# Kernel optimization log

Measured on AMD Instinct MI355X. Metric: run time of the kernel, lower is better.

The kernel has to match this reference:

```python
import jax, jax.numpy as jnp
import numpy as np

D_MODEL = 768
NUM_HEADS = 12
HEAD_DIM = D_MODEL // NUM_HEADS


def setup_inputs() -> dict:
    key = jax.random.key(0)
    ks = jax.random.split(key, 9)
    B, S = 2, 2048
    s = 1.0 / np.sqrt(D_MODEL)
    x = jax.random.normal(ks[0], (B, S, D_MODEL), dtype=jnp.float32)
    Wq = jax.random.normal(ks[1], (D_MODEL, D_MODEL), dtype=jnp.float32) * s
    Wk = jax.random.normal(ks[2], (D_MODEL, D_MODEL), dtype=jnp.float32) * s
    Wv = jax.random.normal(ks[3], (D_MODEL, D_MODEL), dtype=jnp.float32) * s
    Wo = jax.random.normal(ks[4], (D_MODEL, D_MODEL), dtype=jnp.float32) * s
    bq = jax.random.normal(ks[5], (D_MODEL,), dtype=jnp.float32) * 0.01
    bk = jax.random.normal(ks[6], (D_MODEL,), dtype=jnp.float32) * 0.01
    bv = jax.random.normal(ks[7], (D_MODEL,), dtype=jnp.float32) * 0.01
    bo = jax.random.normal(ks[8], (D_MODEL,), dtype=jnp.float32) * 0.01
    return {"x": x, "Wq": Wq, "bq": bq, "Wk": Wk, "bk": bk,
            "Wv": Wv, "bv": bv, "Wo": Wo, "bo": bo}


def reference(x, Wq, bq, Wk, bk, Wv, bv, Wo, bo):
    B, S, _ = x.shape
    # projections; reshape to [B, H, S, Dh]
    def split_heads(t):
        return t.reshape(B, S, NUM_HEADS, HEAD_DIM).transpose(0, 2, 1, 3)
    q = split_heads(x @ Wq + bq)
    k = split_heads(x @ Wk + bk)
    v = split_heads(x @ Wv + bv)
    scale = 1.0 / np.sqrt(HEAD_DIM)
    scores = jnp.einsum("bhqd,bhkd->bhqk", q, k) * scale  # [B,H,S,S]
    attn = jax.nn.softmax(scores, axis=-1)
    # dropout p=0.0 (eval) -> identity
    ctx = jnp.einsum("bhqk,bhkd->bhqd", attn, v)
    ctx = ctx.transpose(0, 2, 1, 3).reshape(B, S, D_MODEL)
    return ctx @ Wo + bo
```

## Files before the change

### kernel.cpp

```cpp
#include <hip/hip_runtime.h>
#include <hip/hip_bf16.h>
#include <hip/hip_fp16.h>

#define D_MODEL 768
#define NHEADS  12
#define HD      64
#define BATCH   2
#define SEQ     2048
#define NTOK    (BATCH*SEQ)
#define NX      ((size_t)NTOK * D_MODEL)
#define NW      ((size_t)D_MODEL * D_MODEL)
#define SC_LOG2 0.18033688f

typedef __attribute__((ext_vector_type(8))) short    short8;
typedef __attribute__((ext_vector_type(8))) _Float16 half8;
typedef __attribute__((ext_vector_type(4))) float    f32x4;

__device__ __forceinline__ float bf2f(short s) {
    union { unsigned u; float f; } c;
    c.u = ((unsigned)(unsigned short)s) << 16;
    return c.f;
}
__device__ __forceinline__ short f2bf(float f) {
    __hip_bfloat16 h = __float2bfloat16(f);
    return *(short*)&h;
}

#ifdef __has_builtin
#if __has_builtin(__builtin_amdgcn_global_load_lds)
#define HAS_GLD 1
#endif
#endif
#ifdef HAS_GLD
#define GLD16(gp, lp) __builtin_amdgcn_global_load_lds( \
    (const __attribute__((address_space(1))) void*)(gp), \
    (__attribute__((address_space(3))) void*)(lp), 16, 0, 0)
#endif

__global__ __launch_bounds__(256) void fused_conv(
        const void* __restrict__ xin,
        const void* __restrict__ w0, const void* __restrict__ w1,
        const void* __restrict__ w2, const void* __restrict__ w3,
        const void* __restrict__ b0, const void* __restrict__ b1,
        const void* __restrict__ b2, const void* __restrict__ b3,
        short* __restrict__ xc, short* __restrict__ wt,
        short* __restrict__ bc, int* __restrict__ flag)
{
    __shared__ int red[256];
    __shared__ float T[64][65];
    const int tid = threadIdx.x;
    const int F = blockIdx.x;

    {
        const short* xs = (const short*)xin;
        int maxe = 0;
#pragma unroll
        for (int u = 0; u < 16; ++u) {
            int e = ((unsigned short)xs[tid * 16 + u] >> 7) & 0xFF;
            maxe = max(maxe, e);
        }
        red[tid] = maxe;
        __syncthreads();
        for (int s = 128; s > 0; s >>= 1) {
            if (tid < s) red[tid] = max(red[tid], red[tid + s]);
            __syncthreads();
        }
    }
    const bool isf = (red[0] > 140);

    if (F < 3072) {
        const int i = F * 256 + tid;
        if (isf) {
            float4 f = ((const float4*)xin)[i];
            short4 o = { f2bf(f.x), f2bf(f.y), f2bf(f.z), f2bf(f.w) };
            ((short4*)xc)[i] = o;
        } else {
            ((short4*)xc)[i] = ((const short4*)xin)[i];
        }
    } else if (F < 3648) {
        const int G = F - 3072;
        const int z = G / 144, rr = G % 144;
        const int k0 = (rr % 12) * 64, n0 = (rr / 12) * 64;
        const void* src = (z == 0) ? w0 : (z == 1) ? w1 : (z == 2) ? w2 : w3;
        const float sc = (z == 0) ? SC_LOG2 : 1.0f;
        const int la = tid & 15, lb = tid >> 4;
#pragma unroll
        for (int u = 0; u < 4; ++u) {
            const int kr = (lb & 3) + 4 * u + 16 * (lb >> 2);
            if (isf) {
                float4 f = *(const float4*)((const float*)src + (size_t)(k0 + kr) * D_MODEL + n0 + la * 4);
                T[kr][la*4+0] = f.x; T[kr][la*4+1] = f.y; T[kr][la*4+2] = f.z; T[kr][la*4+3] = f.w;
            } else {
                short4 s = *(const short4*)((const short*)src + (size_t)(k0 + kr) * D_MODEL + n0 + la * 4);
                T[kr][la*4+0] = bf2f(s.x); T[kr][la*4+1] = bf2f(s.y);
                T[kr][la*4+2] = bf2f(s.z); T[kr][la*4+3] = bf2f(s.w);
            }
        }
        __syncthreads();
#pragma unroll
        for (int u = 0; u < 4; ++u) {
            const int nr = (lb & 3) + 4 * u + 16 * (lb >> 2);
            short4 o = { f2bf(T[la*4+0][nr] * sc), f2bf(T[la*4+1][nr] * sc),
                         f2bf(T[la*4+2][nr] * sc), f2bf(T[la*4+3][nr] * sc) };
            *(short4*)(wt + (size_t)z * NW + (size_t)(n0 + nr) * D_MODEL + k0 + la * 4) = o;
        }
    } else {
        if (tid == 0) *flag = isf ? 1 : 0;
        const void* srcs[4] = { b0, b1, b2, b3 };
        for (int z = 0; z < 4; ++z) {
            const float sc = (z == 0) ? SC_LOG2 : 1.0f;
            for (int i = tid; i < D_MODEL; i += 256) {
                float v = isf ? ((const float*)srcs[z])[i] : bf2f(((const short*)srcs[z])[i]);
                bc[z * D_MODEL + i] = f2bf(v * sc);
            }
        }
    }
}

__global__ __launch_bounds__(256) void qkv_gemm(const short* __restrict__ X,
                                                const short* __restrict__ Wt,
                                                const short* __restrict__ bias,
                                                short* __restrict__ qb,
                                                short* __restrict__ kb,
                                                _Float16* __restrict__ Vt)
{
    __shared__ __align__(16) char shbuf[32768];
    short* Als = (short*)shbuf;
    short* Bls = (short*)(shbuf + 16384);
    _Float16* T = (_Float16*)shbuf;

    const int tid = threadIdx.x;
    const int wave = tid >> 6, lane = tid & 63;
    const int quad = lane >> 4, l16 = lane & 15;
    const int wm = wave & 1, wn = wave >> 1;
    const int m0 = blockIdx.x * 128;
    const int ng = blockIdx.y * 128;

    f32x4 acc[4][4];
#pragma unroll
    for (int nt = 0; nt < 4; ++nt) {
        const float bv = bf2f(bias[ng + wn*64 + nt*16 + l16]);
#pragma unroll
        for (int mt = 0; mt < 4; ++mt) acc[mt][nt] = (f32x4){bv, bv, bv, bv};
    }

    const int row = tid >> 2, ch = (tid & 3) * 8;
#ifdef HAS_GLD
#define QSTAGE(buf, k0) do { \
        GLD16(X  + (size_t)(m0 + row)      * D_MODEL + (k0) + ch, &Als[(buf)*4096 + tid*8]); \
        GLD16(X  + (size_t)(m0 + 64 + row) * D_MODEL + (k0) + ch, &Als[(buf)*4096 + 2048 + tid*8]); \
        GLD16(Wt + (size_t)(ng + row)      * D_MODEL + (k0) + ch, &Bls[(buf)*4096 + tid*8]); \
        GLD16(Wt + (size_t)(ng + 64 + row) * D_MODEL + (k0) + ch, &Bls[(buf)*4096 + 2048 + tid*8]); \
    } while (0)
#else
#define QSTAGE(buf, k0) do { \
        short8 r0 = *(const short8*)(X  + (size_t)(m0 + row)      * D_MODEL + (k0) + ch); \
        short8 r1 = *(const short8*)(X  + (size_t)(m0 + 64 + row) * D_MODEL + (k0) + ch); \
        short8 r2 = *(const short8*)(Wt + (size_t)(ng + row)      * D_MODEL + (k0) + ch); \
        short8 r3 = *(const short8*)(Wt + (size_t)(ng + 64 + row) * D_MODEL + (k0) + ch); \
        *(short8*)&Als[(buf)*4096 + tid*8] = r0;  *(short8*)&Als[(buf)*4096 + 2048 + tid*8] = r1; \
        *(short8*)&Bls[(buf)*4096 + tid*8] = r2;  *(short8*)&Bls[(buf)*4096 + 2048 + tid*8] = r3; \
    } while (0)
#endif

    QSTAGE(0, 0);
    __syncthreads();

    for (int ks = 0; ks < 24; ++ks) {
        const int cur = ks & 1;
        if (ks + 1 < 24) QSTAGE(cur ^ 1, (ks + 1) * 32);

        short8 a[4], b[4];
#pragma unroll
        for (int mt = 0; mt < 4; ++mt)
            a[mt] = *(const short8*)&Als[cur*4096 + (wm*64 + mt*16 + l16) * 32 + quad*8];
#pragma unroll
        for (int nt = 0; nt < 4; ++nt)
            b[nt] = *(const short8*)&Bls[cur*4096 + (wn*64 + nt*16 + l16) * 32 + quad*8];
#pragma unroll
        for (int mt = 0; mt < 4; ++mt)
#pragma unroll
        for (int nt = 0; nt < 4; ++nt)
            acc[mt][nt] = __builtin_amdgcn_mfma_f32_16x16x32_bf16(a[mt], b[nt], acc[mt][nt], 0, 0, 0);

        __syncthreads();
    }
#undef QSTAGE

    const int seg = blockIdx.y / 6;
    if (seg < 2) {
        short* out = seg ? kb : qb;
        const int nl = ng - seg * 768;
#pragma unroll
        for (int mt = 0; mt < 4; ++mt)
#pragma unroll
        for (int nt = 0; nt < 4; ++nt) {
            const int n = nl + wn*64 + nt*16 + l16;
#pragma unroll
            for (int r = 0; r < 4; ++r) {
                const int m = m0 + wm*64 + mt*16 + quad*4 + r;
                out[(size_t)m * D_MODEL + n] = f2bf(acc[mt][nt][r]);
            }
        }
    } else {
        const int batch = m0 >> 11, tokb = m0 & (SEQ - 1);
        for (int pass = 0; pass < 2; ++pass) {
            if (wn == pass) {
#pragma unroll
                for (int nt = 0; nt < 4; ++nt) {
                    const int dim_l = nt*16 + l16;
#pragma unroll
                    for (int mt = 0; mt < 4; ++mt) {
                        const int tok_l = wm*64 + mt*16 + quad*4;
                        union { _Float16 h4[4]; int2 v; } u;
#pragma unroll
                        for (int r = 0; r < 4; ++r) u.h4[r] = (_Float16)acc[mt][nt][r];
                        *(int2*)&T[dim_l * 136 + tok_l] = u.v;
                    }
                }
            }
            __syncthreads();
#pragma unroll
            for (int u = 0; u < 4; ++u) {
                const int slot = tid + u * 256;
                const int drow = slot >> 4, chk = slot & 15;
                int4 val = *(const int4*)&T[drow * 136 + chk * 8];
                const int dim_g = ng - 1536 + pass*64 + drow;
                const int h = dim_g >> 6, d = dim_g & 63;
                *(int4*)(Vt + ((size_t)(batch * NHEADS + h) * HD + d) * SEQ + tokb + chk*8) = val;
            }
            if (pass == 0) __syncthreads();
        }
    }
}

__global__ __launch_bounds__(256) void out_gemm(const short* __restrict__ X,
                                                const short* __restrict__ Wt,
                                                const short* __restrict__ bias,
                                                void* __restrict__ outv,
                                                const int* __restrict__ flag)
{
    __shared__ short Als[2][2048];
    __shared__ short Bls[2][2048];

    const int tid = threadIdx.x;
    const int wave = tid >> 6, lane = tid & 63;
    const int quad = lane >> 4, l16 = lane & 15;
    const int m0 = blockIdx.x * 64;
    const int n0 = blockIdx.y * 64;

    f32x4 acc[4];
#pragma unroll
    for (int nt = 0; nt < 4; ++nt) {
        const float bv = bf2f(bias[n0 + nt*16 + l16]);
        acc[nt] = (f32x4){bv, bv, bv, bv};
    }

    const int row = tid >> 2, ch = (tid & 3) * 8;
#ifdef HAS_GLD
#define OSTAGE(buf, k0) do { \
        GLD16(X  + (size_t)(m0 + row) * D_MODEL + (k0) + ch, &Als[buf][tid*8]); \
        GLD16(Wt + (size_t)(n0 + row) * D_MODEL + (k0) + ch, &Bls[buf][tid*8]); \
    } while (0)
#else
#define OSTAGE(buf, k0) do { \
        short8 r0 = *(const short8*)(X  + (size_t)(m0 + row) * D_MODEL + (k0) + ch); \
        short8 r1 = *(const short8*)(Wt + (size_t)(n0 + row) * D_MODEL + (k0) + ch); \
        *(short8*)&Als[buf][tid*8] = r0; \
        *(short8*)&Bls[buf][tid*8] = r1; \
    } while (0)
#endif

    OSTAGE(0, 0);
    __syncthreads();

    for (int ks = 0; ks < 24; ++ks) {
        const int cur = ks & 1;
        if (ks + 1 < 24) OSTAGE(cur ^ 1, (ks + 1) * 32);

        short8 a = *(const short8*)&Als[cur][(wave*16 + l16) * 32 + quad*8];
#pragma unroll
        for (int nt = 0; nt < 4; ++nt) {
            short8 b = *(const short8*)&Bls[cur][(nt*16 + l16) * 32 + quad*8];
            acc[nt] = __builtin_amdgcn_mfma_f32_16x16x32_bf16(a, b, acc[nt], 0, 0, 0);
        }
        __syncthreads();
    }
#undef OSTAGE

    const bool outf32 = (*flag != 0);
#pragma unroll
    for (int nt = 0; nt < 4; ++nt) {
        const int n = n0 + nt*16 + l16;
#pragma unroll
        for (int r = 0; r < 4; ++r) {
            const int m = m0 + wave*16 + quad*4 + r;
            const size_t idx = (size_t)m * D_MODEL + n;
            if (outf32) ((float*)outv)[idx] = acc[nt][r];
            else        ((short*)outv)[idx] = f2bf(acc[nt][r]);
        }
    }
}

__global__ __launch_bounds__(256) void attn_mfma(const short* __restrict__ q,
                                                 const short* __restrict__ k,
                                                 const _Float16* __restrict__ Vt,
                                                 short* __restrict__ ctx)
{
    __shared__ short    Kls[2][64 * 64];
    __shared__ _Float16 Vls[2][64 * 64];
    __shared__ _Float16 Pls[4][16 * 64];

    const int tid  = threadIdx.x;
    const int wave = tid >> 6, lane = tid & 63;
    const int quad = lane >> 4, l16 = lane & 15;

    const int F = blockIdx.x;
    const int xcd = F & 7, slot = F >> 3;
    const int bh = xcd * 3 + (slot >> 5);
    const int q0 = (slot & 31) * 64;
    const int b = bh / NHEADS, h = bh % NHEADS;
    const size_t bS = (size_t)b * SEQ;
    const int myq = q0 + wave * 16 + l16;

    short8 qf[2];
#pragma unroll
    for (int k0h = 0; k0h < 2; ++k0h)
        qf[k0h] = *(const short8*)(q + (bS + myq) * D_MODEL + h*HD + k0h*32 + quad*8);

    half8 ones;
#pragma unroll
    for (int j = 0; j < 8; ++j) ones[j] = (_Float16)1.0f;

    const int s0 = tid, s1 = tid + 256;
    const int kr0 = s0 >> 3, kc0 = (s0 & 7) ^ (kr0 & 7);
    const int kr1 = s1 >> 3, kc1 = (s1 & 7) ^ (kr1 & 7);
    const short*    kg0 = k  + (bS + kr0) * D_MODEL + h*HD + kc0*8;
    const short*    kg1 = k  + (bS + kr1) * D_MODEL + h*HD + kc1*8;
    const _Float16* vg0 = Vt + ((size_t)bh * HD + kr0) * SEQ + kc0*8;
    const _Float16* vg1 = Vt + ((size_t)bh * HD + kr1) * SEQ + kc1*8;

#ifdef HAS_GLD
#define STAGE(buf, j0) do { \
        GLD16(kg0 + (size_t)(j0) * D_MODEL, &Kls[buf][s0 * 8]); \
        GLD16(kg1 + (size_t)(j0) * D_MODEL, &Kls[buf][s1 * 8]); \
        GLD16(vg0 + (j0),                   &Vls[buf][s0 * 8]); \
        GLD16(vg1 + (j0),                   &Vls[buf][s1 * 8]); \
    } while (0)
#else
#define STAGE(buf, j0) do { \
        short8 a_ = *(const short8*)(kg0 + (size_t)(j0) * D_MODEL); \
        short8 b_ = *(const short8*)(kg1 + (size_t)(j0) * D_MODEL); \
        half8  c_ = *(const half8*)(vg0 + (j0)); \
        half8  d_ = *(const half8*)(vg1 + (j0)); \
        *(short8*)&Kls[buf][s0 * 8] = a_;  *(short8*)&Kls[buf][s1 * 8] = b_; \
        *(half8*)&Vls[buf][s0 * 8] = c_;   *(half8*)&Vls[buf][s1 * 8] = d_; \
    } while (0)
#endif

    float m_ = -1e30f;
    f32x4 lacc = (f32x4){0.f, 0.f, 0.f, 0.f};
    f32x4 o[4];
#pragma unroll
    for (int t = 0; t < 4; ++t) o[t] = (f32x4){0.f, 0.f, 0.f, 0.f};

    STAGE(0, 0);
    __syncthreads();

    for (int jt = 0; jt < SEQ / 64; ++jt) {
        const int cur = jt & 1;
        if (jt + 1 < SEQ / 64) STAGE(cur ^ 1, (jt + 1) * 64);

        f32x4 s4[4];
#pragma unroll
        for (int t = 0; t < 4; ++t) s4[t] = (f32x4){0.f, 0.f, 0.f, 0.f};
#pragma unroll
        for (int k0h = 0; k0h < 2; ++k0h)
#pragma unroll
        for (int t = 0; t < 4; ++t) {
            const int krow = t*16 + l16;
            short8 kf = *(const short8*)&Kls[cur][krow*64 + (((k0h*4 + quad) ^ (krow & 7)) * 8)];
            s4[t] = __builtin_amdgcn_mfma_f32_16x16x32_bf16(kf, qf[k0h], s4[t], 0, 0, 0);
        }

        float mx = s4[0][0];
#pragma unroll
        for (int t = 0; t < 4; ++t)
#pragma unroll
        for (int r = 0; r < 4; ++r) mx = fmaxf(mx, s4[t][r]);
#pragma unroll
        for (int d = 1; d < 64; d <<= 1) mx = fmaxf(mx, __shfl_xor(mx, d));
        const float mn = fmaxf(m_, mx);
        if (__builtin_amdgcn_readfirstlane((int)(mn > m_))) {
            const float al = exp2f(m_ - mn);
#pragma unroll
            for (int t = 0; t < 4; ++t) {
                o[t][0] *= al; o[t][1] *= al; o[t][2] *= al; o[t][3] *= al;
            }
            lacc[0] *= al; lacc[1] *= al; lacc[2] *= al; lacc[3] *= al;
            m_ = mn;
        }

#pragma unroll
        for (int t = 0; t < 4; ++t) {
            union { _Float16 h4[4]; int2 v; } u4;
#pragma unroll
            for (int r = 0; r < 4; ++r) u4.h4[r] = (_Float16)exp2f(s4[t][r] - mn);
            const int c = (t*2 + (quad >> 1)) ^ (l16 & 7);
            *(int2*)&Pls[wave][l16*64 + c*8 + (quad & 1)*4] = u4.v;
        }

#pragma unroll
        for (int k0h = 0; k0h < 2; ++k0h) {
            const int pc = (k0h*4 + quad) ^ (l16 & 7);
            half8 pf = *(half8*)&Pls[wave][l16*64 + pc*8];
            lacc = __builtin_amdgcn_mfma_f32_16x16x32_f16(ones, pf, lacc, 0, 0, 0);
#pragma unroll
            for (int t = 0; t < 4; ++t) {
                const int vrow = t*16 + l16;
                half8 vf = *(const half8*)&Vls[cur][vrow*64 + (((k0h*4 + quad) ^ (vrow & 7)) * 8)];
                o[t] = __builtin_amdgcn_mfma_f32_16x16x32_f16(vf, pf, o[t], 0, 0, 0);
            }
        }

        __syncthreads();
    }

    const float inv = 1.0f / lacc[0];
    const size_t rowp = (bS + myq) * D_MODEL + h*HD;
#pragma unroll
    for (int t = 0; t < 4; ++t) {
        union { short s4v[4]; int2 v; } u4;
#pragma unroll
        for (int r = 0; r < 4; ++r) u4.s4v[r] = f2bf(o[t][r] * inv);
        *(int2*)(ctx + rowp + t*16 + quad*4) = u4.v;
    }
#undef STAGE
}

extern "C" void kernel_launch(void* const* d_in, const int* in_sizes, int n_in,
                              void* d_out, int out_size, void* d_ws, size_t ws_size,
                              hipStream_t stream)
{
    int* flag = (int*)d_ws;
    short* xc = (short*)((char*)d_ws + 64);
    short* Wt = xc + NX;
    short* bc = Wt + 4 * NW;
    short* qb = bc + 4 * D_MODEL;
    short* kb = qb + NX;
    _Float16* Vt = (_Float16*)(kb + NX);
    short* cb = (short*)(Vt + NX);

    fused_conv<<<3649, 256, 0, stream>>>(d_in[0],
                                         d_in[1], d_in[3], d_in[5], d_in[7],
                                         d_in[2], d_in[4], d_in[6], d_in[8],
                                         xc, Wt, bc, flag);

    qkv_gemm<<<dim3(NTOK/128, 2304/128), 256, 0, stream>>>(xc, Wt, bc, qb, kb, Vt);

    attn_mfma<<<768, 256, 0, stream>>>(qb, kb, Vt, cb);

    out_gemm<<<dim3(NTOK/64, D_MODEL/64), 256, 0, stream>>>(cb, Wt + 3*NW, bc + 3*D_MODEL, d_out, flag);
}
```

Baseline: 195.1 us.

## Split key tiles across wave pairs and reuse K/V fragments over two query groups

Each pair of waves now shares 32 queries, and each wave processes half of every 64-key tile, so every K and V fragment read from LDS feeds two MFMAs instead of one. A final merge step rescales the two partial softmax states through shared memory and writes the context rows. The cross-lane max reduction is now skipped when no lane's max rose. The aim is to cut LDS fragment traffic per MFMA. The cost is a cross-wave merge epilogue that reuses the K buffer as float scratch, and that scratch is larger than Kls alone, so it relies on Vls being laid out right after it.

```diff
diff --git a/kernel.cpp b/kernel.cpp
--- a/kernel.cpp
+++ b/kernel.cpp
@@ -302,14 +302,16 @@
     }
 }
 
+#define PROW 40
 __global__ __launch_bounds__(256) void attn_mfma(const short* __restrict__ q,
                                                  const short* __restrict__ k,
                                                  const _Float16* __restrict__ Vt,
                                                  short* __restrict__ ctx)
 {
-    __shared__ short    Kls[2][64 * 64];
-    __shared__ _Float16 Vls[2][64 * 64];
-    __shared__ _Float16 Pls[4][16 * 64];
+    __shared__ short    Kls[2][4096];
+    __shared__ _Float16 Vls[2][4096];
+    __shared__ _Float16 Pw[4][32 * PROW];
+    __shared__ float    Ml[4][32][2];
 
     const int tid  = threadIdx.x;
     const int wave = tid >> 6, lane = tid & 63;
@@ -321,12 +323,18 @@
     const int q0 = (slot & 31) * 64;
     const int b = bh / NHEADS, h = bh % NHEADS;
     const size_t bS = (size_t)b * SEQ;
-    const int myq = q0 + wave * 16 + l16;
-
-    short8 qf[2];
+
+    const int pairq = wave >> 1;
+    const int kh    = wave & 1;
+    const int qbase = q0 + pairq * 32;
+
+    short8 qf[2][2];
+#pragma unroll
+    for (int qg = 0; qg < 2; ++qg)
 #pragma unroll
     for (int k0h = 0; k0h < 2; ++k0h)
-        qf[k0h] = *(const short8*)(q + (bS + myq) * D_MODEL + h*HD + k0h*32 + quad*8);
+        qf[qg][k0h] = *(const short8*)(q + (bS + qbase + qg*16 + l16) * D_MODEL
+                                         + h*HD + k0h*32 + quad*8);
 
     half8 ones;
 #pragma unroll
@@ -359,10 +367,14 @@
 #endif
 
     float m_ = -1e30f;
-    f32x4 lacc = (f32x4){0.f, 0.f, 0.f, 0.f};
-    f32x4 o[4];
-#pragma unroll
-    for (int t = 0; t < 4; ++t) o[t] = (f32x4){0.f, 0.f, 0.f, 0.f};
+    f32x4 lacc[2];
+    f32x4 o[2][4];
+#pragma unroll
+    for (int qg = 0; qg < 2; ++qg) {
+        lacc[qg] = (f32x4){0.f, 0.f, 0.f, 0.f};
+#pragma unroll
+        for (int t = 0; t < 4; ++t) o[qg][t] = (f32x4){0.f, 0.f, 0.f, 0.f};
+    }
 
     STAGE(0, 0);
     __syncthreads();
@@ -371,69 +383,112 @@
         const int cur = jt & 1;
         if (jt + 1 < SEQ / 64) STAGE(cur ^ 1, (jt + 1) * 64);
 
-        f32x4 s4[4];
-#pragma unroll
-        for (int t = 0; t < 4; ++t) s4[t] = (f32x4){0.f, 0.f, 0.f, 0.f};
+        f32x4 s4[2][2];
+#pragma unroll
+        for (int qg = 0; qg < 2; ++qg)
+#pragma unroll
+        for (int t = 0; t < 2; ++t) s4[qg][t] = (f32x4){0.f, 0.f, 0.f, 0.f};
 #pragma unroll
         for (int k0h = 0; k0h < 2; ++k0h)
 #pragma unroll
+        for (int t = 0; t < 2; ++t) {
+            const int krow = kh*32 + t*16 + l16;
+            short8 kf = *(const short8*)&Kls[cur][krow*64 + (((k0h*4 + quad) ^ (krow & 7)) * 8)];
+#pragma unroll
+            for (int qg = 0; qg < 2; ++qg)
+                s4[qg][t] = __builtin_amdgcn_mfma_f32_16x16x32_bf16(kf, qf[qg][k0h], s4[qg][t], 0, 0, 0);
+        }
+
+        float mx = s4[0][0][0];
+#pragma unroll
+        for (int qg = 0; qg < 2; ++qg)
+#pragma unroll
+        for (int t = 0; t < 2; ++t)
+#pragma unroll
+        for (int r = 0; r < 4; ++r) mx = fmaxf(mx, s4[qg][t][r]);
+        if (__any(mx > m_)) {
+#pragma unroll
+            for (int d = 1; d < 64; d <<= 1) mx = fmaxf(mx, __shfl_xor(mx, d));
+            const float mn = fmaxf(m_, mx);
+            const float al = exp2f(m_ - mn);
+#pragma unroll
+            for (int qg = 0; qg < 2; ++qg) {
+#pragma unroll
+                for (int t = 0; t < 4; ++t) {
+                    o[qg][t][0] *= al; o[qg][t][1] *= al;
+                    o[qg][t][2] *= al; o[qg][t][3] *= al;
+                }
+                lacc[qg][0] *= al; lacc[qg][1] *= al;
+                lacc[qg][2] *= al; lacc[qg][3] *= al;
+            }
+            m_ = mn;
+        }
+
+#pragma unroll
+        for (int qg = 0; qg < 2; ++qg)
+#pragma unroll
+        for (int t = 0; t < 2; ++t) {
+            union { _Float16 h4[4]; int2 v; } u4;
+#pragma unroll
+            for (int r = 0; r < 4; ++r) u4.h4[r] = (_Float16)exp2f(s4[qg][t][r] - m_);
+            *(int2*)&Pw[wave][(qg*16 + l16) * PROW + t*16 + quad*4] = u4.v;
+        }
+
+        half8 pf[2];
+#pragma unroll
+        for (int qg = 0; qg < 2; ++qg) {
+            pf[qg] = *(half8*)&Pw[wave][(qg*16 + l16) * PROW + quad*8];
+            lacc[qg] = __builtin_amdgcn_mfma_f32_16x16x32_f16(ones, pf[qg], lacc[qg], 0, 0, 0);
+        }
+#pragma unroll
         for (int t = 0; t < 4; ++t) {
-            const int krow = t*16 + l16;
-            short8 kf = *(const short8*)&Kls[cur][krow*64 + (((k0h*4 + quad) ^ (krow & 7)) * 8)];
-            s4[t] = __builtin_amdgcn_mfma_f32_16x16x32_bf16(kf, qf[k0h], s4[t], 0, 0, 0);
-        }
-
-        float mx = s4[0][0];
+            const int vrow = t*16 + l16;
+            half8 vf = *(const half8*)&Vls[cur][vrow*64 + (((kh*4 + quad) ^ (vrow & 7)) * 8)];
+#pragma unroll
+            for (int qg = 0; qg < 2; ++qg)
+                o[qg][t] = __builtin_amdgcn_mfma_f32_16x16x32_f16(vf, pf[qg], o[qg][t], 0, 0, 0);
+        }
+
+        __syncthreads();
+    }
+
+    float* Ow = (float*)&Kls[0][0];
+#pragma unroll
+    for (int qg = 0; qg < 2; ++qg) {
 #pragma unroll
         for (int t = 0; t < 4; ++t)
-#pragma unroll
-        for (int r = 0; r < 4; ++r) mx = fmaxf(mx, s4[t][r]);
-#pragma unroll
-        for (int d = 1; d < 64; d <<= 1) mx = fmaxf(mx, __shfl_xor(mx, d));
-        const float mn = fmaxf(m_, mx);
-        if (__builtin_amdgcn_readfirstlane((int)(mn > m_))) {
-            const float al = exp2f(m_ - mn);
-#pragma unroll
-            for (int t = 0; t < 4; ++t) {
-                o[t][0] *= al; o[t][1] *= al; o[t][2] *= al; o[t][3] *= al;
-            }
-            lacc[0] *= al; lacc[1] *= al; lacc[2] *= al; lacc[3] *= al;
-            m_ = mn;
-        }
-
-#pragma unroll
-        for (int t = 0; t < 4; ++t) {
-            union { _Float16 h4[4]; int2 v; } u4;
-#pragma unroll
-            for (int r = 0; r < 4; ++r) u4.h4[r] = (_Float16)exp2f(s4[t][r] - mn);
-            const int c = (t*2 + (quad >> 1)) ^ (l16 & 7);
-            *(int2*)&Pls[wave][l16*64 + c*8 + (quad & 1)*4] = u4.v;
-        }
-
-#pragma unroll
-        for (int k0h = 0; k0h < 2; ++k0h) {
-            const int pc = (k0h*4 + quad) ^ (l16 & 7);
-            half8 pf = *(half8*)&Pls[wave][l16*64 + pc*8];
-            lacc = __builtin_amdgcn_mfma_f32_16x16x32_f16(ones, pf, lacc, 0, 0, 0);
-#pragma unroll
-            for (int t = 0; t < 4; ++t) {
-                const int vrow = t*16 + l16;
-                half8 vf = *(const half8*)&Vls[cur][vrow*64 + (((k0h*4 + quad) ^ (vrow & 7)) * 8)];
-                o[t] = __builtin_amdgcn_mfma_f32_16x16x32_f16(vf, pf, o[t], 0, 0, 0);
-            }
-        }
-
-        __syncthreads();
-    }
-
-    const float inv = 1.0f / lacc[0];
-    const size_t rowp = (bS + myq) * D_MODEL + h*HD;
-#pragma unroll
-    for (int t = 0; t < 4; ++t) {
-        union { short s4v[4]; int2 v; } u4;
-#pragma unroll
-        for (int r = 0; r < 4; ++r) u4.s4v[r] = f2bf(o[t][r] * inv);
-        *(int2*)(ctx + rowp + t*16 + quad*4) = u4.v;
+            *(f32x4*)&Ow[(wave*32 + qg*16 + l16) * 64 + t*16 + quad*4] = o[qg][t];
+        if (quad == 0) {
+            Ml[wave][qg*16 + l16][0] = m_;
+            Ml[wave][qg*16 + l16][1] = lacc[qg][0];
+        }
+    }
+    __syncthreads();
+
+    {
+        const int qg2 = tid >> 2;
+        const int seg = tid & 3;
+        const int pr  = qg2 >> 5, ql = qg2 & 31;
+        const int wa = pr*2, wb = wa + 1;
+        const float ma = Ml[wa][ql][0], la = Ml[wa][ql][1];
+        const float mb = Ml[wb][ql][0], lb = Ml[wb][ql][1];
+        const float M = fmaxf(ma, mb);
+        const float sa = exp2f(ma - M), sb = exp2f(mb - M);
+        const float inv = 1.0f / (la * sa + lb * sb);
+        union { short s8[8]; int4 v; } u0, u1;
+#pragma unroll
+        for (int i = 0; i < 4; ++i) {
+            f32x4 oa = *(const f32x4*)&Ow[(wa*32 + ql) * 64 + seg*16 + i*4];
+            f32x4 ob = *(const f32x4*)&Ow[(wb*32 + ql) * 64 + seg*16 + i*4];
+#pragma unroll
+            for (int r = 0; r < 4; ++r) {
+                const short v = f2bf((oa[r] * sa + ob[r] * sb) * inv);
+                if (i < 2) u0.s8[i*4 + r] = v; else u1.s8[(i-2)*4 + r] = v;
+            }
+        }
+        short* cp = ctx + (bS + q0 + qg2) * D_MODEL + h*HD + seg*16;
+        *(int4*)cp = u0.v;
+        *(int4*)(cp + 8) = u1.v;
     }
 #undef STAGE
 }
```

Result: slower. 216.0 us (+10.7%).

## Fuse x fp32-to-bf16 conversion into QKV GEMM A-tile loads

Applied to the files above, without the earlier changes.

Removes the separate x conversion pass from the prep kernel, which shrinks it from 3649 to 577 blocks and drops the xc workspace buffer. The QKV GEMM now reads the raw input, converting fp32 to bf16 in registers when the flag says the input is float, and writes the A tile to LDS after the MFMAs of each step. This avoids a full write and reread of the converted activation. In exchange, each GEMM block rereads fp32 x (twice the bytes) across all 18 N-blocks, and the A tile can no longer use direct global-to-LDS loads.

```diff
diff --git a/kernel.cpp b/kernel.cpp
--- a/kernel.cpp
+++ b/kernel.cpp
@@ -43,8 +43,7 @@
         const void* __restrict__ w2, const void* __restrict__ w3,
         const void* __restrict__ b0, const void* __restrict__ b1,
         const void* __restrict__ b2, const void* __restrict__ b3,
-        short* __restrict__ xc, short* __restrict__ wt,
-        short* __restrict__ bc, int* __restrict__ flag)
+        short* __restrict__ wt, short* __restrict__ bc, int* __restrict__ flag)
 {
     __shared__ int red[256];
     __shared__ float T[64][65];
@@ -68,18 +67,8 @@
     }
     const bool isf = (red[0] > 140);
 
-    if (F < 3072) {
-        const int i = F * 256 + tid;
-        if (isf) {
-            float4 f = ((const float4*)xin)[i];
-            short4 o = { f2bf(f.x), f2bf(f.y), f2bf(f.z), f2bf(f.w) };
-            ((short4*)xc)[i] = o;
-        } else {
-            ((short4*)xc)[i] = ((const short4*)xin)[i];
-        }
-    } else if (F < 3648) {
-        const int G = F - 3072;
-        const int z = G / 144, rr = G % 144;
+    if (F < 576) {
+        const int z = F / 144, rr = F % 144;
         const int k0 = (rr % 12) * 64, n0 = (rr / 12) * 64;
         const void* src = (z == 0) ? w0 : (z == 1) ? w1 : (z == 2) ? w2 : w3;
         const float sc = (z == 0) ? SC_LOG2 : 1.0f;
@@ -117,12 +106,13 @@
     }
 }
 
-__global__ __launch_bounds__(256) void qkv_gemm(const short* __restrict__ X,
+__global__ __launch_bounds__(256) void qkv_gemm(const void* __restrict__ xin,
                                                 const short* __restrict__ Wt,
                                                 const short* __restrict__ bias,
                                                 short* __restrict__ qb,
                                                 short* __restrict__ kb,
-                                                _Float16* __restrict__ Vt)
+                                                _Float16* __restrict__ Vt,
+                                                const int* __restrict__ flag)
 {
     __shared__ __align__(16) char shbuf[32768];
     short* Als = (short*)shbuf;
@@ -135,6 +125,7 @@
     const int wm = wave & 1, wn = wave >> 1;
     const int m0 = blockIdx.x * 128;
     const int ng = blockIdx.y * 128;
+    const bool isf = (*flag != 0);
 
     f32x4 acc[4][4];
 #pragma unroll
@@ -145,30 +136,56 @@
     }
 
     const int row = tid >> 2, ch = (tid & 3) * 8;
+    const float* xf = (const float*)xin;
+    const short* xs = (const short*)xin;
+
+#define ALOAD(a0, a1, k0) do { \
+        if (isf) { \
+            const float* p0 = xf + (size_t)(m0 + row)      * D_MODEL + (k0) + ch; \
+            const float* p1 = xf + (size_t)(m0 + 64 + row) * D_MODEL + (k0) + ch; \
+            float4 f00 = *(const float4*)p0, f01 = *(const float4*)(p0 + 4); \
+            float4 f10 = *(const float4*)p1, f11 = *(const float4*)(p1 + 4); \
+            a0 = (short8){ f2bf(f00.x), f2bf(f00.y), f2bf(f00.z), f2bf(f00.w), \
+                           f2bf(f01.x), f2bf(f01.y), f2bf(f01.z), f2bf(f01.w) }; \
+            a1 = (short8){ f2bf(f10.x), f2bf(f10.y), f2bf(f10.z), f2bf(f10.w), \
+                           f2bf(f11.x), f2bf(f11.y), f2bf(f11.z), f2bf(f11.w) }; \
+        } else { \
+            a0 = *(const short8*)(xs + (size_t)(m0 + row)      * D_MODEL + (k0) + ch); \
+            a1 = *(const short8*)(xs + (size_t)(m0 + 64 + row) * D_MODEL + (k0) + ch); \
+        } \
+    } while (0)
+
 #ifdef HAS_GLD
-#define QSTAGE(buf, k0) do { \
-        GLD16(X  + (size_t)(m0 + row)      * D_MODEL + (k0) + ch, &Als[(buf)*4096 + tid*8]); \
-        GLD16(X  + (size_t)(m0 + 64 + row) * D_MODEL + (k0) + ch, &Als[(buf)*4096 + 2048 + tid*8]); \
+#define BSTAGE(buf, k0) do { \
         GLD16(Wt + (size_t)(ng + row)      * D_MODEL + (k0) + ch, &Bls[(buf)*4096 + tid*8]); \
         GLD16(Wt + (size_t)(ng + 64 + row) * D_MODEL + (k0) + ch, &Bls[(buf)*4096 + 2048 + tid*8]); \
     } while (0)
 #else
-#define QSTAGE(buf, k0) do { \
-        short8 r0 = *(const short8*)(X  + (size_t)(m0 + row)      * D_MODEL + (k0) + ch); \
-        short8 r1 = *(const short8*)(X  + (size_t)(m0 + 64 + row) * D_MODEL + (k0) + ch); \
+#define BSTAGE(buf, k0) do { \
         short8 r2 = *(const short8*)(Wt + (size_t)(ng + row)      * D_MODEL + (k0) + ch); \
         short8 r3 = *(const short8*)(Wt + (size_t)(ng + 64 + row) * D_MODEL + (k0) + ch); \
-        *(short8*)&Als[(buf)*4096 + tid*8] = r0;  *(short8*)&Als[(buf)*4096 + 2048 + tid*8] = r1; \
-        *(short8*)&Bls[(buf)*4096 + tid*8] = r2;  *(short8*)&Bls[(buf)*4096 + 2048 + tid*8] = r3; \
-    } while (0)
-#endif
-
-    QSTAGE(0, 0);
+        *(short8*)&Bls[(buf)*4096 + tid*8] = r2; \
+        *(short8*)&Bls[(buf)*4096 + 2048 + tid*8] = r3; \
+    } while (0)
+#endif
+
+    {
+        short8 a0, a1;
+        ALOAD(a0, a1, 0);
+        BSTAGE(0, 0);
+        *(short8*)&Als[tid*8] = a0;
+        *(short8*)&Als[2048 + tid*8] = a1;
+    }
     __syncthreads();
 
     for (int ks = 0; ks < 24; ++ks) {
-        const int cur = ks & 1;
-        if (ks + 1 < 24) QSTAGE(cur ^ 1, (ks + 1) * 32);
+        const int cur = ks & 1, nxt = cur ^ 1;
+        short8 a0n, a1n;
+        const bool have = (ks + 1 < 24);
+        if (have) {
+            ALOAD(a0n, a1n, (ks + 1) * 32);
+            BSTAGE(nxt, (ks + 1) * 32);
+        }
 
         short8 a[4], b[4];
 #pragma unroll
@@ -183,9 +200,14 @@
         for (int nt = 0; nt < 4; ++nt)
             acc[mt][nt] = __builtin_amdgcn_mfma_f32_16x16x32_bf16(a[mt], b[nt], acc[mt][nt], 0, 0, 0);
 
+        if (have) {
+            *(short8*)&Als[nxt*4096 + tid*8] = a0n;
+            *(short8*)&Als[nxt*4096 + 2048 + tid*8] = a1n;
+        }
         __syncthreads();
     }
-#undef QSTAGE
+#undef ALOAD
+#undef BSTAGE
 
     const int seg = blockIdx.y / 6;
     if (seg < 2) {
@@ -443,20 +465,19 @@
                               hipStream_t stream)
 {
     int* flag = (int*)d_ws;
-    short* xc = (short*)((char*)d_ws + 64);
-    short* Wt = xc + NX;
+    short* Wt = (short*)((char*)d_ws + 64);
     short* bc = Wt + 4 * NW;
     short* qb = bc + 4 * D_MODEL;
     short* kb = qb + NX;
     _Float16* Vt = (_Float16*)(kb + NX);
     short* cb = (short*)(Vt + NX);
 
-    fused_conv<<<3649, 256, 0, stream>>>(d_in[0],
-                                         d_in[1], d_in[3], d_in[5], d_in[7],
-                                         d_in[2], d_in[4], d_in[6], d_in[8],
-                                         xc, Wt, bc, flag);
-
-    qkv_gemm<<<dim3(NTOK/128, 2304/128), 256, 0, stream>>>(xc, Wt, bc, qb, kb, Vt);
+    fused_conv<<<577, 256, 0, stream>>>(d_in[0],
+                                        d_in[1], d_in[3], d_in[5], d_in[7],
+                                        d_in[2], d_in[4], d_in[6], d_in[8],
+                                        Wt, bc, flag);
+
+    qkv_gemm<<<dim3(NTOK/128, 2304/128), 256, 0, stream>>>(d_in[0], Wt, bc, qb, kb, Vt, flag);
 
     attn_mfma<<<768, 256, 0, stream>>>(qb, kb, Vt, cb);
 
```

New measurement: 206.7 us. 1.06x slower.
